# Optimization experiments

Hardware: AMD Instinct MI355X
Metric: run time of the kernel (lower is better)

Reference implementation:

```python
import jax, jax.numpy as jnp
import numpy as np
from math import sqrt

B, S, E, H = 2, 2048, 1024, 16

def setup_inputs() -> dict:
    key = jax.random.key(0)
    k1, k2, k3, k4, k5 = jax.random.split(key, 5)
    bound_in = 1.0 / sqrt(E)
    return {
        "inputs": jax.random.normal(k1, (B, S, E), dtype=jnp.float32),
        "W_in": jax.random.uniform(k2, (3 * E, E), dtype=jnp.float32, minval=-bound_in, maxval=bound_in),
        "b_in": jax.random.uniform(k3, (3 * E,), dtype=jnp.float32, minval=-bound_in, maxval=bound_in),
        "W_out": jax.random.uniform(k4, (E, E), dtype=jnp.float32, minval=-bound_in, maxval=bound_in),
        "b_out": jax.random.uniform(k5, (E,), dtype=jnp.float32, minval=-bound_in, maxval=bound_in),
    }

def reference(inputs, W_in, b_in, W_out, b_out):
    # Eval-mode forward (dropout is identity when not training).
    b, s, e = inputs.shape
    hd = e // H
    qkv = jnp.einsum('bse,fe->bsf', inputs, W_in) + b_in  # [B,S,3E]
    q, k, v = jnp.split(qkv, 3, axis=-1)
    # [B,S,E] -> [B,H,S,hd]
    to_heads = lambda t: t.reshape(b, s, H, hd).transpose(0, 2, 1, 3)
    q, k, v = to_heads(q), to_heads(k), to_heads(v)
    scores = jnp.einsum('bhqd,bhkd->bhqk', q, k) / jnp.sqrt(jnp.float32(hd))
    causal = jnp.tril(jnp.ones((s, s), dtype=bool))
    scores = jnp.where(causal, scores, -jnp.inf)
    attn = jax.nn.softmax(scores, axis=-1)  # stable max-subtract softmax, same math
    out = jnp.einsum('bhqk,bhkd->bhqd', attn, v)  # [B,H,S,hd]
    out = out.transpose(0, 2, 1, 3).reshape(b, s, e)
    return jnp.einsum('bse,fe->bsf', out, W_out) + b_out
```

## Files before the change

### kernel.cpp

```cpp
#include <hip/hip_runtime.h>
#include <hip/hip_bf16.h>
#include <stdint.h>

#define SS 2048
#define EE 1024
#define HH 16
#define HD 64

#define QSCALE 0.1803368801111137f

typedef __attribute__((ext_vector_type(8))) short short8;
typedef __attribute__((ext_vector_type(4))) float f32x4;

__device__ __forceinline__ short f2bf(float f) {
  union { float f; uint32_t u; } x; x.f = f;
  uint32_t r = x.u + 0x7fffu + ((x.u >> 16) & 1u);
  return (short)(r >> 16);
}

__device__ __forceinline__ uint32_t pk_bf16(float a, float b) {
#if __has_builtin(__builtin_amdgcn_cvt_pk_bf16_f32)
  typedef __attribute__((ext_vector_type(2))) __bf16 bf16x2_t;
  union { bf16x2_t v; uint32_t u; } x;
  x.v = __builtin_amdgcn_cvt_pk_bf16_f32(a, b);
  return x.u;
#else
  return (uint32_t)(uint16_t)f2bf(a) | ((uint32_t)(uint16_t)f2bf(b) << 16);
#endif
}

#if __has_builtin(__builtin_amdgcn_exp2f)
#define EXP2F __builtin_amdgcn_exp2f
#else
#define EXP2F exp2f
#endif

__device__ __forceinline__ void async_cp16(const void* g, void* l) {
  __builtin_amdgcn_global_load_lds((const __attribute__((address_space(1))) void*)g,
                                   (__attribute__((address_space(3))) void*)l, 16, 0, 0);
}

#define N4_X  1048576
#define N4_W1 786432
#define N4_W2 262144
#define N4_ALL (N4_X + N4_W1 + N4_W2)
__global__ __launch_bounds__(256) void cvt_all(
    const float* __restrict__ x, const float* __restrict__ w1,
    const float* __restrict__ w2,
    short* __restrict__ xb, short* __restrict__ w1b, short* __restrict__ w2b)
{
  for (int i = blockIdx.x * 256 + threadIdx.x; i < N4_ALL; i += 2048 * 256) {
    const float* src; short* dst; int off;
    if (i < N4_X)            { src = x;  dst = xb;  off = i; }
    else if (i < N4_X+N4_W1) { src = w1; dst = w1b; off = i - N4_X; }
    else                     { src = w2; dst = w2b; off = i - N4_X - N4_W1; }
    float4 v = *(const float4*)&src[(size_t)off * 4];
    uint2 pk;
    pk.x = pk_bf16(v.x, v.y);
    pk.y = pk_bf16(v.z, v.w);
    *(uint2*)&dst[(size_t)off * 4] = pk;
  }
}

__global__ __launch_bounds__(256) void gemm_qkv(
    const short* __restrict__ A, const short* __restrict__ Bw,
    const float* __restrict__ bias,
    short* __restrict__ qw, short* __restrict__ kw, short* __restrict__ vw,
    int M, int N, int K)
{
  __shared__ short smem[17408];
  const int tid = threadIdx.x;
  const int lane = tid & 63;
  const int wv = tid >> 6;
  const int wm = (wv >> 1) * 64;
  const int wn = (wv & 1) * 64;
  const int t = lane >> 4;
  const int lr = lane & 15;
  const int bm = blockIdx.y * 128;
  const int bn = blockIdx.x * 128;

  f32x4 acc[4][4];
  #pragma unroll
  for (int i = 0; i < 4; ++i)
    #pragma unroll
    for (int j = 0; j < 4; ++j) acc[i][j] = (f32x4){0.f, 0.f, 0.f, 0.f};

  auto stage = [&](int buf, int k0) {
    short* sA = smem + buf * 8192;
    short* sB = smem + buf * 8192 + 4096;
    #pragma unroll
    for (int it = 0; it < 2; ++it) {
      int c = it * 256 + wv * 64 + lane;
      int row = c >> 2;
      int ch = (c & 3) * 8;
      async_cp16(&A[(size_t)(bm + row) * K + k0 + ch],
                 (char*)sA + (size_t)(it * 256 + wv * 64) * 16);
      async_cp16(&Bw[(size_t)(bn + row) * K + k0 + ch],
                 (char*)sB + (size_t)(it * 256 + wv * 64) * 16);
    }
  };

  const bool isV = (bn >= 2048);
  const bool isQ = (bn < 1024);
  const int nk = K >> 5;
  stage(0, 0);
  __syncthreads();

  if (isV) {
    float bvv[4];
    #pragma unroll
    for (int j = 0; j < 4; ++j) bvv[j] = bias[bn + wn + j*16 + lr];

    for (int k = 0; k < nk; ++k) {
      if (k + 1 < nk) stage((k + 1) & 1, (k + 1) << 5);
      const short* cA = smem + (k & 1) * 8192;
      const short* cB = smem + (k & 1) * 8192 + 4096;
      short8 af[4], bfr[4];
      #pragma unroll
      for (int i = 0; i < 4; ++i) af[i] = *(const short8*)&cA[(wm + i*16 + lr)*32 + t*8];
      #pragma unroll
      for (int j = 0; j < 4; ++j) bfr[j] = *(const short8*)&cB[(wn + j*16 + lr)*32 + t*8];
      #pragma unroll
      for (int i = 0; i < 4; ++i)
        #pragma unroll
        for (int j = 0; j < 4; ++j)
          acc[i][j] = __builtin_amdgcn_mfma_f32_16x16x32_bf16(af[i], bfr[j], acc[i][j], 0, 0, 0);
      __syncthreads();
    }

    short* vx = smem;
    int b_ = bm >> 11;
    int s0 = bm & 2047;
    #pragma unroll
    for (int i = 0; i < 4; ++i) {
      int row0 = wm + i*16 + t*4;
      #pragma unroll
      for (int j = 0; j < 4; ++j) {
        int cl = wn + j*16 + lr;
        float bv = bvv[j];
        uint2 pw;
        pw.x = pk_bf16(acc[i][j][0] + bv, acc[i][j][1] + bv);
        pw.y = pk_bf16(acc[i][j][2] + bv, acc[i][j][3] + bv);
        *(uint2*)&vx[cl*136 + row0] = pw;
      }
    }
    __syncthreads();
    int h0 = (bn - 2048) >> 6;
    #pragma unroll
    for (int it = 0; it < 8; ++it) {
      int cc = it * 256 + tid;
      int cl = cc >> 4;
      int ck = cc & 15;
      int h = h0 + (cl >> 6);
      int d = cl & 63;
      int f = ck >> 2, tt = ck & 3;
      const short* src = &vx[cl*136 + 32*f + 4*tt];
      uint2 lo = *(const uint2*)src;
      uint2 hi = *(const uint2*)(src + 16);
      uint4 val; val.x = lo.x; val.y = lo.y; val.z = hi.x; val.w = hi.y;
      *(uint4*)&vw[((size_t)(b_*HH + h)*HD + d)*SS + s0 + ck*8] = val;
    }
  } else {
    float4 bq[4];
    #pragma unroll
    for (int j = 0; j < 4; ++j) bq[j] = *(const float4*)&bias[bn + wn + j*16 + t*4];

    for (int k = 0; k < nk; ++k) {
      if (k + 1 < nk) stage((k + 1) & 1, (k + 1) << 5);
      const short* cA = smem + (k & 1) * 8192;
      const short* cB = smem + (k & 1) * 8192 + 4096;
      short8 af[4], bfr[4];
      #pragma unroll
      for (int i = 0; i < 4; ++i) af[i] = *(const short8*)&cA[(wm + i*16 + lr)*32 + t*8];
      #pragma unroll
      for (int j = 0; j < 4; ++j) bfr[j] = *(const short8*)&cB[(wn + j*16 + lr)*32 + t*8];
      #pragma unroll
      for (int i = 0; i < 4; ++i)
        #pragma unroll
        for (int j = 0; j < 4; ++j)
          acc[i][j] = __builtin_amdgcn_mfma_f32_16x16x32_bf16(bfr[j], af[i], acc[i][j], 0, 0, 0);
      __syncthreads();
    }

    short* vx = smem;
    int b_ = bm >> 11;
    int s0 = bm & 2047;
    #pragma unroll
    for (int j = 0; j < 4; ++j) {
      int col0 = wn + j*16 + t*4;
      float4 bv4 = bq[j];
      #pragma unroll
      for (int i = 0; i < 4; ++i) {
        int row = wm + i*16 + lr;
        float v0 = acc[i][j][0] + bv4.x;
        float v1 = acc[i][j][1] + bv4.y;
        float v2 = acc[i][j][2] + bv4.z;
        float v3 = acc[i][j][3] + bv4.w;
        if (isQ) { v0 *= QSCALE; v1 *= QSCALE; v2 *= QSCALE; v3 *= QSCALE; }
        uint2 pw;
        pw.x = pk_bf16(v0, v1);
        pw.y = pk_bf16(v2, v3);
        *(uint2*)&vx[row*136 + col0] = pw;
      }
    }
    __syncthreads();
    short* dst = isQ ? qw : kw;
    int h0 = (bn & 1023) >> 6;
    #pragma unroll
    for (int it = 0; it < 8; ++it) {
      int cc = it * 256 + tid;
      int row = cc >> 4;
      int ck = cc & 15;
      int h = h0 + (ck >> 3);
      int d0 = (ck & 7) * 8;
      *(uint4*)&dst[((size_t)(b_*HH + h)*SS + s0 + row)*HD + d0] =
          *(const uint4*)&vx[row*136 + ck*8];
    }
  }
}

__global__ __launch_bounds__(256) void gemm_out(
    const short* __restrict__ A, const short* __restrict__ Bw,
    const float* __restrict__ bias,
    float* __restrict__ C,
    int M, int N, int K)
{
  __shared__ short smem[12288];
  const int tid = threadIdx.x;
  const int lane = tid & 63;
  const int wv = tid >> 6;
  const int wm = (wv >> 1) * 32;
  const int wn = (wv & 1) * 64;
  const int t = lane >> 4;
  const int lr = lane & 15;
  const int bm = blockIdx.y * 64;
  const int bn = blockIdx.x * 128;

  f32x4 acc[2][4];
  #pragma unroll
  for (int i = 0; i < 2; ++i)
    #pragma unroll
    for (int j = 0; j < 4; ++j) acc[i][j] = (f32x4){0.f, 0.f, 0.f, 0.f};

  float bvo[4];
  #pragma unroll
  for (int j = 0; j < 4; ++j) bvo[j] = bias[bn + wn + j*16 + lr];

  auto stage = [&](int buf, int k0) {
    short* sA = smem + buf * 6144;
    short* sB = smem + buf * 6144 + 2048;
    {
      int c = wv * 64 + lane;
      int row = c >> 2;
      int ch = (c & 3) * 8;
      async_cp16(&A[(size_t)(bm + row) * K + k0 + ch],
                 (char*)sA + (size_t)(wv * 64) * 16);
    }
    #pragma unroll
    for (int it = 0; it < 2; ++it) {
      int c = it * 256 + wv * 64 + lane;
      int row = c >> 2;
      int ch = (c & 3) * 8;
      async_cp16(&Bw[(size_t)(bn + row) * K + k0 + ch],
                 (char*)sB + (size_t)(it * 256 + wv * 64) * 16);
    }
  };

  const int nk = K >> 5;
  stage(0, 0);
  __syncthreads();

  for (int k = 0; k < nk; ++k) {
    if (k + 1 < nk) stage((k + 1) & 1, (k + 1) << 5);
    const short* cA = smem + (k & 1) * 6144;
    const short* cB = smem + (k & 1) * 6144 + 2048;
    short8 af[2], bfr[4];
    #pragma unroll
    for (int i = 0; i < 2; ++i) af[i] = *(const short8*)&cA[(wm + i*16 + lr)*32 + t*8];
    #pragma unroll
    for (int j = 0; j < 4; ++j) bfr[j] = *(const short8*)&cB[(wn + j*16 + lr)*32 + t*8];
    #pragma unroll
    for (int i = 0; i < 2; ++i)
      #pragma unroll
      for (int j = 0; j < 4; ++j)
        acc[i][j] = __builtin_amdgcn_mfma_f32_16x16x32_bf16(af[i], bfr[j], acc[i][j], 0, 0, 0);
    __syncthreads();
  }

  #pragma unroll
  for (int i = 0; i < 2; ++i) {
    int row0 = bm + wm + i*16 + t*4;
    #pragma unroll
    for (int j = 0; j < 4; ++j) {
      int col = bn + wn + j*16 + lr;
      float bv = bvo[j];
      #pragma unroll
      for (int r = 0; r < 4; ++r)
        C[(size_t)(row0 + r) * N + col] = acc[i][j][r] + bv;
    }
  }
}

template<int MODE, typename TA>
__global__ __launch_bounds__(256) void gemm_bt(
    const TA* __restrict__ A, const float* __restrict__ Bw,
    const float* __restrict__ bias,
    float* __restrict__ C,
    short* __restrict__ qw, short* __restrict__ kw, short* __restrict__ vw,
    int M, int N, int K)
{
  __shared__ short sA[128*32];
  __shared__ short sB[128*32];
  const int tid = threadIdx.x;
  const int lane = tid & 63;
  const int wv = tid >> 6;
  const int wm = (wv >> 1) * 64;
  const int wn = (wv & 1) * 64;
  const int t = lane >> 4;
  const int lr = lane & 15;
  const int bm = blockIdx.y * 128;
  const int bn = blockIdx.x * 128;

  f32x4 acc[4][4];
  #pragma unroll
  for (int i = 0; i < 4; ++i)
    #pragma unroll
    for (int j = 0; j < 4; ++j) acc[i][j] = (f32x4){0.f, 0.f, 0.f, 0.f};

  for (int k0 = 0; k0 < K; k0 += 32) {
    __syncthreads();
    if constexpr (sizeof(TA) == 4) {
      #pragma unroll
      for (int it = 0; it < 4; ++it) {
        int c = it * 256 + tid;
        int row = c >> 3, ch = (c & 7) * 4;
        float4 va = *(const float4*)&A[(size_t)(bm + row)*K + k0 + ch];
        uint2 pk; pk.x = pk_bf16(va.x, va.y); pk.y = pk_bf16(va.z, va.w);
        *(uint2*)&sA[row*32 + ch] = pk;
      }
    } else {
      #pragma unroll
      for (int it = 0; it < 2; ++it) {
        int c = it * 256 + tid;
        int row = c >> 2, ch = (c & 3) * 8;
        *(uint4*)&sA[row*32 + ch] = *(const uint4*)&A[(size_t)(bm + row)*K + k0 + ch];
      }
    }
    #pragma unroll
    for (int it = 0; it < 4; ++it) {
      int c = it * 256 + tid;
      int row = c >> 3, ch = (c & 7) * 4;
      float4 vb = *(const float4*)&Bw[(size_t)(bn + row)*K + k0 + ch];
      uint2 pk; pk.x = pk_bf16(vb.x, vb.y); pk.y = pk_bf16(vb.z, vb.w);
      *(uint2*)&sB[row*32 + ch] = pk;
    }
    __syncthreads();
    short8 af[4], bfr[4];
    #pragma unroll
    for (int i = 0; i < 4; ++i) af[i] = *(const short8*)&sA[(wm + i*16 + lr)*32 + t*8];
    #pragma unroll
    for (int j = 0; j < 4; ++j) bfr[j] = *(const short8*)&sB[(wn + j*16 + lr)*32 + t*8];
    #pragma unroll
    for (int i = 0; i < 4; ++i)
      #pragma unroll
      for (int j = 0; j < 4; ++j)
        acc[i][j] = __builtin_amdgcn_mfma_f32_16x16x32_bf16(af[i], bfr[j], acc[i][j], 0, 0, 0);
  }

  #pragma unroll
  for (int i = 0; i < 4; ++i) {
    int row0 = bm + wm + i*16 + t*4;
    #pragma unroll
    for (int j = 0; j < 4; ++j) {
      int col = bn + wn + j*16 + lr;
      float bv = bias[col];
      #pragma unroll
      for (int r = 0; r < 4; ++r) {
        float v = acc[i][j][r] + bv;
        int rr = row0 + r;
        if (MODE == 0) {
          C[(size_t)rr * N + col] = v;
        } else {
          int which = col >> 10;
          int e = col & 1023;
          int h = e >> 6, d = e & 63;
          int b_ = rr >> 11, s = rr & 2047;
          if (which == 0)
            qw[((size_t)(b_*HH + h)*SS + s)*HD + d] = f2bf(v * QSCALE);
          else if (which == 1)
            kw[((size_t)(b_*HH + h)*SS + s)*HD + d] = f2bf(v);
          else {
            int k7 = s & 127;
            int sp = (k7 & 0x60) | ((k7 & 0x0C) << 1) | ((k7 & 0x10) >> 2) | (k7 & 3);
            vw[((size_t)(b_*HH + h)*HD + d)*SS + (s & ~127) + sp] = f2bf(v);
          }
        }
      }
    }
  }
}

__global__ __launch_bounds__(512) void attn_kernel(
    const short* __restrict__ Q, const short* __restrict__ K,
    const short* __restrict__ Vt, short* __restrict__ O)
{
  __shared__ short sK[2][128*64];
  __shared__ short sV[2][64*128];
  const int tid = threadIdx.x;
  const int lane = tid & 63;
  const int w = tid >> 6;
  const int t = lane >> 4;
  const int lr = lane & 15;
  const int blk = blockIdx.x;
  const int qt = (blk < 256) ? (blk >> 5) : (15 - ((blk - 256) >> 5));
  const int bh = blk & 31;
  const int b = bh >> 4, h = bh & 15;
  const short* Qb = Q  + (size_t)bh * SS * HD;
  const short* Kb = K  + (size_t)bh * SS * HD;
  const short* Vb = Vt + (size_t)bh * HD * SS;
  const int qrow0 = qt * 128 + w * 16;

  auto stage = [&](int buf, int kb) {
    #pragma unroll
    for (int it2 = 0; it2 < 2; ++it2) {
      int s = it2 * 512 + tid;
      int krow = s >> 3;
      int kcc = (s & 7) ^ (krow & 7);
      async_cp16(&Kb[(size_t)(kb + krow) * HD + kcc * 8],
                 (char*)sK[buf] + (size_t)(it2 * 512 + w * 64) * 16);
      int d = s >> 4;
      int vcc = (s & 15) ^ (d & 15);
      async_cp16(&Vb[(size_t)d * SS + kb + vcc * 8],
                 (char*)sV[buf] + (size_t)(it2 * 512 + w * 64) * 16);
    }
  };

  short8 qf[2];
  #pragma unroll
  for (int st = 0; st < 2; ++st)
    qf[st] = *(const short8*)&Qb[(size_t)(qrow0 + lr) * HD + st*32 + t*8];

  f32x4 o[4];
  #pragma unroll
  for (int jd = 0; jd < 4; ++jd) o[jd] = (f32x4){0.f, 0.f, 0.f, 0.f};
  float l = 0.f;

  const int niter = qt + 1;
  stage(0, 0);
  __syncthreads();
  int cur = 0;

  #pragma unroll 1
  for (int it = 0; it < niter - 1; ++it) {
    const int kb = it * 128;
    stage(cur ^ 1, kb + 128);
    const short* sKc = sK[cur];
    const short* sVc = sV[cur];

    f32x4 sc[8];
    #pragma unroll
    for (int c = 0; c < 8; ++c) sc[c] = (f32x4){0.f,0.f,0.f,0.f};
    __builtin_amdgcn_s_setprio(1);
    #pragma unroll
    for (int c = 0; c < 8; ++c) {
      int krow = c*16 + lr;
      #pragma unroll
      for (int st = 0; st < 2; ++st) {
        int slot = krow*8 + ((st*4 + t) ^ (lr & 7));
        short8 kf = *(const short8*)&sKc[slot*8];
        sc[c] = __builtin_amdgcn_mfma_f32_16x16x32_bf16(kf, qf[st], sc[c], 0, 0, 0);
      }
    }
    __builtin_amdgcn_s_setprio(0);

    float rs0 = 0.f, rs1 = 0.f, rs2 = 0.f, rs3 = 0.f;
    #pragma unroll
    for (int c = 0; c < 8; ++c) {
      sc[c][0] = EXP2F(sc[c][0]);
      sc[c][1] = EXP2F(sc[c][1]);
      sc[c][2] = EXP2F(sc[c][2]);
      sc[c][3] = EXP2F(sc[c][3]);
      rs0 += sc[c][0];
      rs1 += sc[c][1];
      rs2 += sc[c][2];
      rs3 += sc[c][3];
    }
    float rs = (rs0 + rs1) + (rs2 + rs3);
    rs += __shfl_xor(rs, 16);
    rs += __shfl_xor(rs, 32);
    l += rs;

    __builtin_amdgcn_s_setprio(1);
    #pragma unroll
    for (int f = 0; f < 4; ++f) {
      union { uint32_t u[4]; short8 s8; } up;
      up.u[0] = pk_bf16(sc[2*f  ][0], sc[2*f  ][1]);
      up.u[1] = pk_bf16(sc[2*f  ][2], sc[2*f  ][3]);
      up.u[2] = pk_bf16(sc[2*f+1][0], sc[2*f+1][1]);
      up.u[3] = pk_bf16(sc[2*f+1][2], sc[2*f+1][3]);
      short8 pf = up.s8;
      #pragma unroll
      for (int jd = 0; jd < 4; ++jd) {
        int d = jd*16 + lr;
        int vslot = d*16 + ((f*4 + t) ^ lr);
        short8 vf = *(const short8*)&sVc[vslot*8];
        o[jd] = __builtin_amdgcn_mfma_f32_16x16x32_bf16(vf, pf, o[jd], 0, 0, 0);
      }
    }
    __builtin_amdgcn_s_setprio(0);

    __syncthreads();
    cur ^= 1;
  }

  {
    const short* sKc = sK[cur];
    const short* sVc = sV[cur];

    f32x4 sc[8];
    #pragma unroll
    for (int c = 0; c < 8; ++c) sc[c] = (f32x4){0.f,0.f,0.f,0.f};
    __builtin_amdgcn_s_setprio(1);
    #pragma unroll
    for (int c = 0; c < 8; ++c) {
      if (c > w) continue;
      int krow = c*16 + lr;
      #pragma unroll
      for (int st = 0; st < 2; ++st) {
        int slot = krow*8 + ((st*4 + t) ^ (lr & 7));
        short8 kf = *(const short8*)&sKc[slot*8];
        sc[c] = __builtin_amdgcn_mfma_f32_16x16x32_bf16(kf, qf[st], sc[c], 0, 0, 0);
      }
    }
    __builtin_amdgcn_s_setprio(0);

    #pragma unroll
    for (int c = 0; c < 8; ++c) {
      if (c != w) continue;
      #pragma unroll
      for (int r = 0; r < 4; ++r)
        if (4*t + r > lr) sc[c][r] = -1e30f;
    }

    float rs0 = 0.f, rs1 = 0.f, rs2 = 0.f, rs3 = 0.f;
    #pragma unroll
    for (int c = 0; c < 8; ++c) {
      if (c > w) continue;
      sc[c][0] = EXP2F(sc[c][0]);
      sc[c][1] = EXP2F(sc[c][1]);
      sc[c][2] = EXP2F(sc[c][2]);
      sc[c][3] = EXP2F(sc[c][3]);
      rs0 += sc[c][0];
      rs1 += sc[c][1];
      rs2 += sc[c][2];
      rs3 += sc[c][3];
    }
    float rs = (rs0 + rs1) + (rs2 + rs3);
    rs += __shfl_xor(rs, 16);
    rs += __shfl_xor(rs, 32);
    l += rs;

    __builtin_amdgcn_s_setprio(1);
    #pragma unroll
    for (int f = 0; f < 4; ++f) {
      if (f > (w >> 1)) continue;
      union { uint32_t u[4]; short8 s8; } up;
      up.u[0] = pk_bf16(sc[2*f  ][0], sc[2*f  ][1]);
      up.u[1] = pk_bf16(sc[2*f  ][2], sc[2*f  ][3]);
      up.u[2] = pk_bf16(sc[2*f+1][0], sc[2*f+1][1]);
      up.u[3] = pk_bf16(sc[2*f+1][2], sc[2*f+1][3]);
      short8 pf = up.s8;
      #pragma unroll
      for (int jd = 0; jd < 4; ++jd) {
        int d = jd*16 + lr;
        int vslot = d*16 + ((f*4 + t) ^ lr);
        short8 vf = *(const short8*)&sVc[vslot*8];
        o[jd] = __builtin_amdgcn_mfma_f32_16x16x32_bf16(vf, pf, o[jd], 0, 0, 0);
      }
    }
    __builtin_amdgcn_s_setprio(0);
  }

  float linv = 1.0f / l;
  size_t rowoff = ((size_t)(b * SS + qrow0 + lr)) * EE + h * HD;
  #pragma unroll
  for (int jd = 0; jd < 4; ++jd) {
    uint2 pw;
    pw.x = pk_bf16(o[jd][0] * linv, o[jd][1] * linv);
    pw.y = pk_bf16(o[jd][2] * linv, o[jd][3] * linv);
    *(uint2*)&O[rowoff + jd*16 + t*4] = pw;
  }
}

extern "C" void kernel_launch(void* const* d_in, const int* in_sizes, int n_in,
                              void* d_out, int out_size, void* d_ws, size_t ws_size,
                              hipStream_t stream) {
  const float* X     = (const float*)d_in[0];
  const float* W_in  = (const float*)d_in[1];
  const float* b_in  = (const float*)d_in[2];
  const float* W_out = (const float*)d_in[3];
  const float* b_out = (const float*)d_in[4];
  float* out = (float*)d_out;

  char* ws = (char*)d_ws;
  const size_t MB = 1024 * 1024;
  const int M = 2 * SS;

  if (ws_size >= 48 * MB) {
    short* Xb   = (short*)(ws);
    short* Wb1  = (short*)(ws + 8  * MB);
    short* Wb2  = (short*)(ws + 14 * MB);
    short* q_ws = (short*)(ws + 16 * MB);
    short* k_ws = (short*)(ws + 24 * MB);
    short* v_ws = (short*)(ws + 32 * MB);
    short* attn = (short*)(ws + 40 * MB);

    cvt_all<<<2048, 256, 0, stream>>>(X, W_in, W_out, Xb, Wb1, Wb2);
    gemm_qkv<<<dim3(24, 32), 256, 0, stream>>>(
        Xb, Wb1, b_in, q_ws, k_ws, v_ws, M, 3 * EE, EE);
    attn_kernel<<<dim3(512), 512, 0, stream>>>(q_ws, k_ws, v_ws, attn);
    gemm_out<<<dim3(8, 64), 256, 0, stream>>>(
        attn, Wb2, b_out, out, M, EE, EE);
  } else {
    short* q_ws = (short*)(ws);
    short* k_ws = (short*)(ws + 8  * MB);
    short* v_ws = (short*)(ws + 16 * MB);
    short* attn = (short*)(ws + 24 * MB);

    gemm_bt<1, float><<<dim3(24, 32), 256, 0, stream>>>(
        X, W_in, b_in, nullptr, q_ws, k_ws, v_ws, M, 3 * EE, EE);
    attn_kernel<<<dim3(512), 512, 0, stream>>>(q_ws, k_ws, v_ws, attn);
    gemm_bt<0, short><<<dim3(8, 32), 256, 0, stream>>>(
        attn, W_out, b_out, out, nullptr, nullptr, nullptr, M, EE, EE);
  }
}
```

Baseline: 176.3 us.

## Switch attention to 32x32x16 MFMA with split-KV warps and LDS reduction

Rewrites the attention kernel to use 32x32x16 bf16 MFMA instead of 16x16x32. Each group of 4 waves covers 32 query rows, and the two halves of the block each take half of the 128-key tile. The V permutation in the QKV projection is changed to match the new fragment layout, which also turns the V transpose readout into a single 16-byte LDS load. Partial outputs and row sums from the two halves are combined through shared memory at the end. The aim is fewer MFMA and LDS instructions per tile, at the cost of higher register pressure under launch_bounds(512,4) and an extra reduction step.

```diff
diff --git a/kernel.cpp b/kernel.cpp
--- a/kernel.cpp
+++ b/kernel.cpp
@@ -11,6 +11,7 @@
 
 typedef __attribute__((ext_vector_type(8))) short short8;
 typedef __attribute__((ext_vector_type(4))) float f32x4;
+typedef __attribute__((ext_vector_type(16))) float f32x16;
 
 __device__ __forceinline__ short f2bf(float f) {
   union { float f; uint32_t u; } x; x.f = f;
@@ -134,6 +135,9 @@
     #pragma unroll
     for (int i = 0; i < 4; ++i) {
       int row0 = wm + i*16 + t*4;
+      int b4 = (row0 >> 2) & 7;
+      int pb = (b4 & 4) | ((b4 & 1) << 1) | ((b4 >> 1) & 1);
+      int prow = (row0 & ~31) | (pb << 2);
       #pragma unroll
       for (int j = 0; j < 4; ++j) {
         int cl = wn + j*16 + lr;
@@ -141,7 +145,7 @@
         uint2 pw;
         pw.x = pk_bf16(acc[i][j][0] + bv, acc[i][j][1] + bv);
         pw.y = pk_bf16(acc[i][j][2] + bv, acc[i][j][3] + bv);
-        *(uint2*)&vx[cl*136 + row0] = pw;
+        *(uint2*)&vx[cl*136 + prow] = pw;
       }
     }
     __syncthreads();
@@ -153,12 +157,8 @@
       int ck = cc & 15;
       int h = h0 + (cl >> 6);
       int d = cl & 63;
-      int f = ck >> 2, tt = ck & 3;
-      const short* src = &vx[cl*136 + 32*f + 4*tt];
-      uint2 lo = *(const uint2*)src;
-      uint2 hi = *(const uint2*)(src + 16);
-      uint4 val; val.x = lo.x; val.y = lo.y; val.z = hi.x; val.w = hi.y;
-      *(uint4*)&vw[((size_t)(b_*HH + h)*HD + d)*SS + s0 + ck*8] = val;
+      *(uint4*)&vw[((size_t)(b_*HH + h)*HD + d)*SS + s0 + ck*8] =
+          *(const uint4*)&vx[cl*136 + ck*8];
     }
   } else {
     float4 bq[4];
@@ -391,7 +391,13 @@
             kw[((size_t)(b_*HH + h)*SS + s)*HD + d] = f2bf(v);
           else {
             int k7 = s & 127;
-            int sp = (k7 & 0x60) | ((k7 & 0x0C) << 1) | ((k7 & 0x10) >> 2) | (k7 & 3);
+            int t32 = k7 & 96;
+            int kv32 = k7 & 31;
+            int f16 = kv32 & 16;
+            int rem = kv32 & 15;
+            int hh = (rem >> 2) & 1;
+            int jj = (rem & 3) | ((rem >> 3) << 2);
+            int sp = t32 | f16 | (hh << 3) | jj;
             vw[((size_t)(b_*HH + h)*HD + d)*SS + (s & ~127) + sp] = f2bf(v);
           }
         }
@@ -400,7 +406,7 @@
   }
 }
 
-__global__ __launch_bounds__(512) void attn_kernel(
+__global__ __launch_bounds__(512, 4) void attn_kernel(
     const short* __restrict__ Q, const short* __restrict__ K,
     const short* __restrict__ Vt, short* __restrict__ O)
 {
@@ -409,8 +415,10 @@
   const int tid = threadIdx.x;
   const int lane = tid & 63;
   const int w = tid >> 6;
-  const int t = lane >> 4;
-  const int lr = lane & 15;
+  const int g = w & 3;
+  const int hf = w >> 2;
+  const int lq = lane & 31;
+  const int hi = lane >> 5;
   const int blk = blockIdx.x;
   const int qt = (blk < 256) ? (blk >> 5) : (15 - ((blk - 256) >> 5));
   const int bh = blk & 31;
@@ -418,7 +426,7 @@
   const short* Qb = Q  + (size_t)bh * SS * HD;
   const short* Kb = K  + (size_t)bh * SS * HD;
   const short* Vb = Vt + (size_t)bh * HD * SS;
-  const int qrow0 = qt * 128 + w * 16;
+  const int qrow0 = qt * 128 + g * 32;
 
   auto stage = [&](int buf, int kb) {
     #pragma unroll
@@ -435,14 +443,13 @@
     }
   };
 
-  short8 qf[2];
+  short8 qf[4];
   #pragma unroll
-  for (int st = 0; st < 2; ++st)
-    qf[st] = *(const short8*)&Qb[(size_t)(qrow0 + lr) * HD + st*32 + t*8];
-
-  f32x4 o[4];
-  #pragma unroll
-  for (int jd = 0; jd < 4; ++jd) o[jd] = (f32x4){0.f, 0.f, 0.f, 0.f};
+  for (int ds = 0; ds < 4; ++ds)
+    qf[ds] = *(const short8*)&Qb[(size_t)(qrow0 + lq) * HD + ds*16 + hi*8];
+
+  f32x16 o0 = (f32x16)(0.0f);
+  f32x16 o1 = (f32x16)(0.0f);
   float l = 0.f;
 
   const int niter = qt + 1;
@@ -452,62 +459,58 @@
 
   #pragma unroll 1
   for (int it = 0; it < niter - 1; ++it) {
-    const int kb = it * 128;
-    stage(cur ^ 1, kb + 128);
+    stage(cur ^ 1, (it + 1) * 128);
     const short* sKc = sK[cur];
     const short* sVc = sV[cur];
 
-    f32x4 sc[8];
-    #pragma unroll
-    for (int c = 0; c < 8; ++c) sc[c] = (f32x4){0.f,0.f,0.f,0.f};
-    __builtin_amdgcn_s_setprio(1);
-    #pragma unroll
-    for (int c = 0; c < 8; ++c) {
-      int krow = c*16 + lr;
-      #pragma unroll
-      for (int st = 0; st < 2; ++st) {
-        int slot = krow*8 + ((st*4 + t) ^ (lr & 7));
+    #pragma unroll
+    for (int tp = 0; tp < 2; ++tp) {
+      const int tau = 2*hf + tp;
+      f32x16 sc = (f32x16)(0.0f);
+      __builtin_amdgcn_s_setprio(1);
+      #pragma unroll
+      for (int ds = 0; ds < 4; ++ds) {
+        int krow = tau*32 + lq;
+        int slot = krow*8 + ((ds*2 + hi) ^ (krow & 7));
         short8 kf = *(const short8*)&sKc[slot*8];
-        sc[c] = __builtin_amdgcn_mfma_f32_16x16x32_bf16(kf, qf[st], sc[c], 0, 0, 0);
-      }
-    }
-    __builtin_amdgcn_s_setprio(0);
-
-    float rs0 = 0.f, rs1 = 0.f, rs2 = 0.f, rs3 = 0.f;
-    #pragma unroll
-    for (int c = 0; c < 8; ++c) {
-      sc[c][0] = EXP2F(sc[c][0]);
-      sc[c][1] = EXP2F(sc[c][1]);
-      sc[c][2] = EXP2F(sc[c][2]);
-      sc[c][3] = EXP2F(sc[c][3]);
-      rs0 += sc[c][0];
-      rs1 += sc[c][1];
-      rs2 += sc[c][2];
-      rs3 += sc[c][3];
-    }
-    float rs = (rs0 + rs1) + (rs2 + rs3);
-    rs += __shfl_xor(rs, 16);
-    rs += __shfl_xor(rs, 32);
-    l += rs;
-
-    __builtin_amdgcn_s_setprio(1);
-    #pragma unroll
-    for (int f = 0; f < 4; ++f) {
-      union { uint32_t u[4]; short8 s8; } up;
-      up.u[0] = pk_bf16(sc[2*f  ][0], sc[2*f  ][1]);
-      up.u[1] = pk_bf16(sc[2*f  ][2], sc[2*f  ][3]);
-      up.u[2] = pk_bf16(sc[2*f+1][0], sc[2*f+1][1]);
-      up.u[3] = pk_bf16(sc[2*f+1][2], sc[2*f+1][3]);
-      short8 pf = up.s8;
-      #pragma unroll
-      for (int jd = 0; jd < 4; ++jd) {
-        int d = jd*16 + lr;
-        int vslot = d*16 + ((f*4 + t) ^ lr);
-        short8 vf = *(const short8*)&sVc[vslot*8];
-        o[jd] = __builtin_amdgcn_mfma_f32_16x16x32_bf16(vf, pf, o[jd], 0, 0, 0);
-      }
-    }
-    __builtin_amdgcn_s_setprio(0);
+        sc = __builtin_amdgcn_mfma_f32_32x32x16_bf16(kf, qf[ds], sc, 0, 0, 0);
+      }
+      __builtin_amdgcn_s_setprio(0);
+
+      float rs0=0.f, rs1=0.f, rs2=0.f, rs3=0.f;
+      #pragma unroll
+      for (int r = 0; r < 16; r += 4) {
+        sc[r+0] = EXP2F(sc[r+0]); rs0 += sc[r+0];
+        sc[r+1] = EXP2F(sc[r+1]); rs1 += sc[r+1];
+        sc[r+2] = EXP2F(sc[r+2]); rs2 += sc[r+2];
+        sc[r+3] = EXP2F(sc[r+3]); rs3 += sc[r+3];
+      }
+      l += (rs0 + rs1) + (rs2 + rs3);
+
+      __builtin_amdgcn_s_setprio(1);
+      #pragma unroll
+      for (int f = 0; f < 2; ++f) {
+        union { uint32_t u[4]; short8 s8; } up;
+        up.u[0] = pk_bf16(sc[8*f+0], sc[8*f+1]);
+        up.u[1] = pk_bf16(sc[8*f+2], sc[8*f+3]);
+        up.u[2] = pk_bf16(sc[8*f+4], sc[8*f+5]);
+        up.u[3] = pk_bf16(sc[8*f+6], sc[8*f+7]);
+        short8 pf = up.s8;
+        {
+          int d0 = lq;
+          int slot = d0*16 + ((tau*4 + f*2 + hi) ^ (d0 & 15));
+          short8 vf = *(const short8*)&sVc[slot*8];
+          o0 = __builtin_amdgcn_mfma_f32_32x32x16_bf16(vf, pf, o0, 0, 0, 0);
+        }
+        {
+          int d1 = 32 + lq;
+          int slot = d1*16 + ((tau*4 + f*2 + hi) ^ (d1 & 15));
+          short8 vf = *(const short8*)&sVc[slot*8];
+          o1 = __builtin_amdgcn_mfma_f32_32x32x16_bf16(vf, pf, o1, 0, 0, 0);
+        }
+      }
+      __builtin_amdgcn_s_setprio(0);
+    }
 
     __syncthreads();
     cur ^= 1;
@@ -516,79 +519,110 @@
   {
     const short* sKc = sK[cur];
     const short* sVc = sV[cur];
-
-    f32x4 sc[8];
-    #pragma unroll
-    for (int c = 0; c < 8; ++c) sc[c] = (f32x4){0.f,0.f,0.f,0.f};
-    __builtin_amdgcn_s_setprio(1);
-    #pragma unroll
-    for (int c = 0; c < 8; ++c) {
-      if (c > w) continue;
-      int krow = c*16 + lr;
-      #pragma unroll
-      for (int st = 0; st < 2; ++st) {
-        int slot = krow*8 + ((st*4 + t) ^ (lr & 7));
+    const bool act0 = (2*hf)     <= g;
+    const bool act1 = (2*hf + 1) <= g;
+    const bool eq0  = (2*hf)     == g;
+    const bool eq1  = (2*hf + 1) == g;
+
+    #pragma unroll
+    for (int tp = 0; tp < 2; ++tp) {
+      const bool act = tp ? act1 : act0;
+      const bool eq  = tp ? eq1  : eq0;
+      if (!act) continue;
+      const int tau = 2*hf + tp;
+      f32x16 sc = (f32x16)(0.0f);
+      __builtin_amdgcn_s_setprio(1);
+      #pragma unroll
+      for (int ds = 0; ds < 4; ++ds) {
+        int krow = tau*32 + lq;
+        int slot = krow*8 + ((ds*2 + hi) ^ (krow & 7));
         short8 kf = *(const short8*)&sKc[slot*8];
-        sc[c] = __builtin_amdgcn_mfma_f32_16x16x32_bf16(kf, qf[st], sc[c], 0, 0, 0);
-      }
-    }
-    __builtin_amdgcn_s_setprio(0);
-
-    #pragma unroll
-    for (int c = 0; c < 8; ++c) {
-      if (c != w) continue;
-      #pragma unroll
-      for (int r = 0; r < 4; ++r)
-        if (4*t + r > lr) sc[c][r] = -1e30f;
-    }
-
-    float rs0 = 0.f, rs1 = 0.f, rs2 = 0.f, rs3 = 0.f;
-    #pragma unroll
-    for (int c = 0; c < 8; ++c) {
-      if (c > w) continue;
-      sc[c][0] = EXP2F(sc[c][0]);
-      sc[c][1] = EXP2F(sc[c][1]);
-      sc[c][2] = EXP2F(sc[c][2]);
-      sc[c][3] = EXP2F(sc[c][3]);
-      rs0 += sc[c][0];
-      rs1 += sc[c][1];
-      rs2 += sc[c][2];
-      rs3 += sc[c][3];
-    }
-    float rs = (rs0 + rs1) + (rs2 + rs3);
-    rs += __shfl_xor(rs, 16);
-    rs += __shfl_xor(rs, 32);
-    l += rs;
-
-    __builtin_amdgcn_s_setprio(1);
-    #pragma unroll
-    for (int f = 0; f < 4; ++f) {
-      if (f > (w >> 1)) continue;
-      union { uint32_t u[4]; short8 s8; } up;
-      up.u[0] = pk_bf16(sc[2*f  ][0], sc[2*f  ][1]);
-      up.u[1] = pk_bf16(sc[2*f  ][2], sc[2*f  ][3]);
-      up.u[2] = pk_bf16(sc[2*f+1][0], sc[2*f+1][1]);
-      up.u[3] = pk_bf16(sc[2*f+1][2], sc[2*f+1][3]);
-      short8 pf = up.s8;
-      #pragma unroll
-      for (int jd = 0; jd < 4; ++jd) {
-        int d = jd*16 + lr;
-        int vslot = d*16 + ((f*4 + t) ^ lr);
-        short8 vf = *(const short8*)&sVc[vslot*8];
-        o[jd] = __builtin_amdgcn_mfma_f32_16x16x32_bf16(vf, pf, o[jd], 0, 0, 0);
-      }
-    }
-    __builtin_amdgcn_s_setprio(0);
-  }
-
-  float linv = 1.0f / l;
-  size_t rowoff = ((size_t)(b * SS + qrow0 + lr)) * EE + h * HD;
-  #pragma unroll
-  for (int jd = 0; jd < 4; ++jd) {
-    uint2 pw;
-    pw.x = pk_bf16(o[jd][0] * linv, o[jd][1] * linv);
-    pw.y = pk_bf16(o[jd][2] * linv, o[jd][3] * linv);
-    *(uint2*)&O[rowoff + jd*16 + t*4] = pw;
+        sc = __builtin_amdgcn_mfma_f32_32x32x16_bf16(kf, qf[ds], sc, 0, 0, 0);
+      }
+      __builtin_amdgcn_s_setprio(0);
+
+      if (eq) {
+        #pragma unroll
+        for (int r = 0; r < 16; ++r) {
+          int kvl = (r & 3) + 8*(r >> 2) + 4*hi;
+          if (kvl > lq) sc[r] = -1e30f;
+        }
+      }
+
+      float rs0=0.f, rs1=0.f, rs2=0.f, rs3=0.f;
+      #pragma unroll
+      for (int r = 0; r < 16; r += 4) {
+        sc[r+0] = EXP2F(sc[r+0]); rs0 += sc[r+0];
+        sc[r+1] = EXP2F(sc[r+1]); rs1 += sc[r+1];
+        sc[r+2] = EXP2F(sc[r+2]); rs2 += sc[r+2];
+        sc[r+3] = EXP2F(sc[r+3]); rs3 += sc[r+3];
+      }
+      l += (rs0 + rs1) + (rs2 + rs3);
+
+      __builtin_amdgcn_s_setprio(1);
+      #pragma unroll
+      for (int f = 0; f < 2; ++f) {
+        union { uint32_t u[4]; short8 s8; } up;
+        up.u[0] = pk_bf16(sc[8*f+0], sc[8*f+1]);
+        up.u[1] = pk_bf16(sc[8*f+2], sc[8*f+3]);
+        up.u[2] = pk_bf16(sc[8*f+4], sc[8*f+5]);
+        up.u[3] = pk_bf16(sc[8*f+6], sc[8*f+7]);
+        short8 pf = up.s8;
+        {
+          int d0 = lq;
+          int slot = d0*16 + ((tau*4 + f*2 + hi) ^ (d0 & 15));
+          short8 vf = *(const short8*)&sVc[slot*8];
+          o0 = __builtin_amdgcn_mfma_f32_32x32x16_bf16(vf, pf, o0, 0, 0, 0);
+        }
+        {
+          int d1 = 32 + lq;
+          int slot = d1*16 + ((tau*4 + f*2 + hi) ^ (d1 & 15));
+          short8 vf = *(const short8*)&sVc[slot*8];
+          o1 = __builtin_amdgcn_mfma_f32_32x32x16_bf16(vf, pf, o1, 0, 0, 0);
+        }
+      }
+      __builtin_amdgcn_s_setprio(0);
+    }
+  }
+
+  l += __shfl_xor(l, 32);
+
+  float* fx = (float*)&sK[0][0];
+  float* fl = (float*)&sV[0][0];
+
+  __syncthreads();
+  {
+    float* reg = fx + (size_t)(g*2 + (1 - hf)) * 1024;
+    if (hf == 0) {
+      #pragma unroll
+      for (int i = 0; i < 16; ++i) reg[i*64 + lane] = o1[i];
+    } else {
+      #pragma unroll
+      for (int i = 0; i < 16; ++i) reg[i*64 + lane] = o0[i];
+    }
+    if (lane < 32) fl[w*32 + lq] = l;
+  }
+  __syncthreads();
+  {
+    float lp = fl[(g + 4*(1 - hf))*32 + lq];
+    float linv = 1.0f / (l + lp);
+    float* reg = fx + (size_t)(g*2 + hf) * 1024;
+    float ov[16];
+    if (hf == 0) {
+      #pragma unroll
+      for (int i = 0; i < 16; ++i) ov[i] = (o0[i] + reg[i*64 + lane]) * linv;
+    } else {
+      #pragma unroll
+      for (int i = 0; i < 16; ++i) ov[i] = (o1[i] + reg[i*64 + lane]) * linv;
+    }
+    size_t rowoff = ((size_t)(b * SS + qrow0 + lq)) * EE + h * HD + hf*32 + hi*4;
+    #pragma unroll
+    for (int grp = 0; grp < 4; ++grp) {
+      uint2 pw;
+      pw.x = pk_bf16(ov[grp*4+0], ov[grp*4+1]);
+      pw.y = pk_bf16(ov[grp*4+2], ov[grp*4+3]);
+      *(uint2*)&O[rowoff + grp*8] = pw;
+    }
   }
 }
 
```

Result: slower. 191.7 us (+8.7%).
